# Kernel optimization log

Hardware: AMD Instinct MI355X
Metric: run time of the kernel (lower is better)

## Reference

```python
import jax, jax.numpy as jnp
import numpy as np

EPS = 1e-3  # Keras BatchNormalization default epsilon
ROWS = 14


def _lstm_step(h, c, x, W, U, b, act):
    # Keras gate order: i, f, g(cell), o
    z = x @ W + h @ U + b
    i, f, g, o = jnp.split(z, 4, axis=-1)
    c = jax.nn.sigmoid(f) * c + jax.nn.sigmoid(i) * act(g)
    h = jax.nn.sigmoid(o) * act(c)
    return h, c


def _lstm(xs, W, U, b, act):
    # xs: [B, T, F] -> (last_h, last_c), zero initial state
    B = xs.shape[0]
    D = U.shape[0]
    h0 = jnp.zeros((B, D), xs.dtype)
    c0 = jnp.zeros((B, D), xs.dtype)

    def step(carry, x):
        h, c = _lstm_step(carry[0], carry[1], x, W, U, b, act)
        return (h, c), h

    (h, c), hs = jax.lax.scan(step, (h0, c0), jnp.swapaxes(xs, 0, 1))
    return jnp.swapaxes(hs, 0, 1), h, c


def _bn(x, gamma, beta):
    # training-mode batchnorm over all axes but the last (channel) axis
    axes = tuple(range(x.ndim - 1))
    mean = jnp.mean(x, axis=axes)
    var = jnp.var(x, axis=axes)
    return (x - mean) * jax.lax.rsqrt(var + EPS) * gamma + beta


def setup_inputs() -> dict:
    key = jax.random.key(0)
    B, T, F = 65536, 32, 16
    D = 8   # lstm_forward_dims = output_dims * 2
    Do = 4  # lstm_backward_dims = output_dims
    ks = jax.random.split(key, 10)
    p = lambda k, shp: (0.1 * jax.random.normal(k, shp)).astype(jnp.float32)
    return {
        "noise_seed": jax.random.normal(ks[0], (B, T, F), dtype=jnp.float32),
        "W0": p(ks[1], (F, 4 * D)), "U0": p(ks[2], (D, 4 * D)), "b0": jnp.zeros((4 * D,), jnp.float32),
        "gamma_h": jnp.ones((D,), jnp.float32), "beta_h": jnp.zeros((D,), jnp.float32),
        "gamma_c": jnp.ones((D,), jnp.float32), "beta_c": jnp.zeros((D,), jnp.float32),
        "W1": p(ks[3], (D, 4 * D)), "U1": p(ks[4], (D, 4 * D)), "b1": jnp.zeros((4 * D,), jnp.float32),
        "gamma3": jnp.ones((D,), jnp.float32), "beta3": jnp.zeros((D,), jnp.float32),
        "W2": p(ks[5], (D, 4 * Do)), "U2": p(ks[6], (Do, 4 * Do)), "b2": jnp.zeros((4 * Do,), jnp.float32),
        "training": 1,
    }


def reference(noise_seed, W0, U0, b0, gamma_h, beta_h, gamma_c, beta_c,
              W1, U1, b1, gamma3, beta3, W2, U2, b2, training):
    # init LSTM (tanh activation), keep final states
    _, h, c = _lstm(noise_seed, W0, U0, b0, jnp.tanh)
    h = _bn(h, gamma_h, beta_h)
    c = _bn(c, gamma_c, beta_c)

    def step(carry, _):
        h, c = carry
        h2, c2 = _lstm_step(h, c, h, W1, U1, b1, jax.nn.relu)
        return (h2, c2), h2

    _, hs = jax.lax.scan(step, (h, c), None, length=ROWS)  # [ROWS, B, D]
    bars = jnp.swapaxes(hs[::-1], 0, 1)                    # reversed, [B, ROWS, D]
    bars = _bn(bars, gamma3, beta3)

    # backward LSTM (relu activation), return_sequences
    out, _, _ = _lstm(bars, W2, U2, b2, jax.nn.relu)       # [B, ROWS, Do]
    return out
```

## Files before the change

kernel.cpp:

```cpp
#include <hip/hip_runtime.h>
#include <hip/hip_bf16.h>

#define EPSV 1e-3f

__device__ __forceinline__ float rcp_fast(float x){ return __builtin_amdgcn_rcpf(x); }
__device__ __forceinline__ float sigm(float x){
    x = fminf(fmaxf(x, -30.f), 30.f);
    return rcp_fast(1.f + __expf(-x));
}
__device__ __forceinline__ float tanh_fast(float x){
    x = fminf(fmaxf(x, -15.f), 15.f);
    float e = __expf(2.f * x);
    return 1.f - 2.f * rcp_fast(e + 1.f);
}

template<int K>
__device__ __forceinline__ float bc8(float v){
    return __int_as_float(__builtin_amdgcn_ds_swizzle(__float_as_int(v), (K << 5) | 0x18));
}
#define BC8_ALL(dst, src) do { \
    dst[0]=bc8<0>(src); dst[1]=bc8<1>(src); dst[2]=bc8<2>(src); dst[3]=bc8<3>(src); \
    dst[4]=bc8<4>(src); dst[5]=bc8<5>(src); dst[6]=bc8<6>(src); dst[7]=bc8<7>(src); } while(0)

__global__ __launch_bounds__(256) void k1_lstm0(
    const float* __restrict__ noise, const float* __restrict__ W0,
    const float* __restrict__ U0, const float* __restrict__ b0,
    float* __restrict__ Hbuf, float* __restrict__ Cbuf, double* __restrict__ stats1)
{
    const int tid = threadIdx.x;
    const int d = tid & 7;
    const size_t b = (size_t)blockIdx.x * 32 + (tid >> 3);

    float w0c[16][4], u0c[8][4], b0v[4];
    #pragma unroll
    for (int g = 0; g < 4; ++g) b0v[g] = b0[8*g + d];
    #pragma unroll
    for (int f = 0; f < 16; ++f)
        #pragma unroll
        for (int g = 0; g < 4; ++g) w0c[f][g] = W0[f*32 + 8*g + d];
    #pragma unroll
    for (int e = 0; e < 8; ++e)
        #pragma unroll
        for (int g = 0; g < 4; ++g) u0c[e][g] = U0[e*32 + 8*g + d];

    const float4* __restrict__ xrow = reinterpret_cast<const float4*>(noise + b * 512);
    float h = 0.f, c = 0.f;
    #pragma unroll 2
    for (int t = 0; t < 32; ++t){
        float4 q0 = xrow[t*4+0], q1 = xrow[t*4+1], q2 = xrow[t*4+2], q3 = xrow[t*4+3];
        float hall[8]; BC8_ALL(hall, h);
        const float x[16] = {q0.x,q0.y,q0.z,q0.w, q1.x,q1.y,q1.z,q1.w,
                             q2.x,q2.y,q2.z,q2.w, q3.x,q3.y,q3.z,q3.w};
        float z[4] = {b0v[0], b0v[1], b0v[2], b0v[3]};
        #pragma unroll
        for (int f = 0; f < 16; ++f)
            #pragma unroll
            for (int g = 0; g < 4; ++g) z[g] = fmaf(x[f], w0c[f][g], z[g]);
        #pragma unroll
        for (int e = 0; e < 8; ++e)
            #pragma unroll
            for (int g = 0; g < 4; ++g) z[g] = fmaf(hall[e], u0c[e][g], z[g]);
        c = sigm(z[1])*c + sigm(z[0])*tanh_fast(z[2]);
        h = sigm(z[3])*tanh_fast(c);
    }
    Hbuf[(size_t)blockIdx.x*256 + tid] = h;
    Cbuf[(size_t)blockIdx.x*256 + tid] = c;

    float v0 = h, v1 = h*h, v2 = c, v3 = c*c;
    v0 += __shfl_down(v0,32); v0 += __shfl_down(v0,16); v0 += __shfl_down(v0,8);
    v1 += __shfl_down(v1,32); v1 += __shfl_down(v1,16); v1 += __shfl_down(v1,8);
    v2 += __shfl_down(v2,32); v2 += __shfl_down(v2,16); v2 += __shfl_down(v2,8);
    v3 += __shfl_down(v3,32); v3 += __shfl_down(v3,16); v3 += __shfl_down(v3,8);
    __shared__ float red[4][4][8];
    const int w = tid >> 6;
    if ((tid & 63) < 8){ red[0][w][d]=v0; red[1][w][d]=v1; red[2][w][d]=v2; red[3][w][d]=v3; }
    __syncthreads();
    if (tid < 32){
        const int s = tid >> 3, dd = tid & 7;
        float acc = red[s][0][dd] + red[s][1][dd] + red[s][2][dd] + red[s][3][dd];
        atomicAdd(stats1 + s*8 + dd, (double)acc);
    }
}

__global__ __launch_bounds__(256) void k2_ar(
    const float* __restrict__ Hbuf, const float* __restrict__ Cbuf,
    const double* __restrict__ stats1,
    const float* __restrict__ gamma_h, const float* __restrict__ beta_h,
    const float* __restrict__ gamma_c, const float* __restrict__ beta_c,
    const float* __restrict__ W1, const float* __restrict__ U1, const float* __restrict__ b1,
    double* __restrict__ stats3, int B)
{
    const int tid = threadIdx.x;
    const int d = tid & 7;
    const double invB = 1.0 / (double)B;
    const float meanH = (float)(stats1[d]      * invB);
    const float eH2   = (float)(stats1[8 + d]  * invB);
    const float meanC = (float)(stats1[16 + d] * invB);
    const float eC2   = (float)(stats1[24 + d] * invB);
    const float aH = gamma_h[d] * rsqrtf(eH2 - meanH*meanH + EPSV);
    const float aC = gamma_c[d] * rsqrtf(eC2 - meanC*meanC + EPSV);
    const float bH = beta_h[d] - meanH*aH;
    const float bC = beta_c[d] - meanC*aC;
    float h = fmaf(Hbuf[(size_t)blockIdx.x*256 + tid], aH, bH);
    float c = fmaf(Cbuf[(size_t)blockIdx.x*256 + tid], aC, bC);

    float wc[8][4], bcv[4];
    #pragma unroll
    for (int g = 0; g < 4; ++g) bcv[g] = b1[8*g + d];
    #pragma unroll
    for (int e = 0; e < 8; ++e)
        #pragma unroll
        for (int g = 0; g < 4; ++g) wc[e][g] = W1[e*32 + 8*g + d] + U1[e*32 + 8*g + d];

    float s1 = 0.f, s2 = 0.f;
    #pragma unroll
    for (int r = 0; r < 14; ++r){
        float hall[8]; BC8_ALL(hall, h);
        float z[4] = {bcv[0], bcv[1], bcv[2], bcv[3]};
        #pragma unroll
        for (int e = 0; e < 8; ++e)
            #pragma unroll
            for (int g = 0; g < 4; ++g) z[g] = fmaf(hall[e], wc[e][g], z[g]);
        c = sigm(z[1])*c + sigm(z[0])*fmaxf(z[2], 0.f);
        h = sigm(z[3])*fmaxf(c, 0.f);
        s1 += h; s2 = fmaf(h, h, s2);
    }
    s1 += __shfl_down(s1,32); s1 += __shfl_down(s1,16); s1 += __shfl_down(s1,8);
    s2 += __shfl_down(s2,32); s2 += __shfl_down(s2,16); s2 += __shfl_down(s2,8);
    __shared__ float red[2][4][8];
    const int w = tid >> 6;
    if ((tid & 63) < 8){ red[0][w][d] = s1; red[1][w][d] = s2; }
    __syncthreads();
    if (tid < 16){
        const int s = tid >> 3, dd = tid & 7;
        float acc = red[s][0][dd] + red[s][1][dd] + red[s][2][dd] + red[s][3][dd];
        atomicAdd(stats3 + s*8 + dd, (double)acc);
    }
}

__global__ __launch_bounds__(256) void k3_out(
    const float* __restrict__ Hbuf, const float* __restrict__ Cbuf,
    const double* __restrict__ stats1, const double* __restrict__ stats3,
    const float* __restrict__ gamma_h, const float* __restrict__ beta_h,
    const float* __restrict__ gamma_c, const float* __restrict__ beta_c,
    const float* __restrict__ W1, const float* __restrict__ U1, const float* __restrict__ b1,
    const float* __restrict__ gamma3, const float* __restrict__ beta3,
    const float* __restrict__ W2, const float* __restrict__ U2, const float* __restrict__ b2,
    float* __restrict__ out, int B)
{
    const int tid = threadIdx.x;
    const int d = tid & 7;
    const double invB = 1.0 / (double)B;
    const float meanH = (float)(stats1[d]      * invB);
    const float eH2   = (float)(stats1[8 + d]  * invB);
    const float meanC = (float)(stats1[16 + d] * invB);
    const float eC2   = (float)(stats1[24 + d] * invB);
    const float aH = gamma_h[d] * rsqrtf(eH2 - meanH*meanH + EPSV);
    const float aC = gamma_c[d] * rsqrtf(eC2 - meanC*meanC + EPSV);
    const float bH = beta_h[d] - meanH*aH;
    const float bC = beta_c[d] - meanC*aC;
    float h = fmaf(Hbuf[(size_t)blockIdx.x*256 + tid], aH, bH);
    float c = fmaf(Cbuf[(size_t)blockIdx.x*256 + tid], aC, bC);

    float wc[8][4], bcv[4];
    #pragma unroll
    for (int g = 0; g < 4; ++g) bcv[g] = b1[8*g + d];
    #pragma unroll
    for (int e = 0; e < 8; ++e)
        #pragma unroll
        for (int g = 0; g < 4; ++g) wc[e][g] = W1[e*32 + 8*g + d] + U1[e*32 + 8*g + d];

    float barh[14];
    #pragma unroll
    for (int r = 0; r < 14; ++r){
        float hall[8]; BC8_ALL(hall, h);
        float z[4] = {bcv[0], bcv[1], bcv[2], bcv[3]};
        #pragma unroll
        for (int e = 0; e < 8; ++e)
            #pragma unroll
            for (int g = 0; g < 4; ++g) z[g] = fmaf(hall[e], wc[e][g], z[g]);
        c = sigm(z[1])*c + sigm(z[0])*fmaxf(z[2], 0.f);
        h = sigm(z[3])*fmaxf(c, 0.f);
        barh[r] = h;
    }
    const double invN = 1.0 / ((double)B * 14.0);
    const float mean3 = (float)(stats3[d]     * invN);
    const float e32   = (float)(stats3[8 + d] * invN);
    const float a3 = gamma3[d] * rsqrtf(e32 - mean3*mean3 + EPSV);
    const float b3 = beta3[d] - mean3*a3;
    #pragma unroll
    for (int r = 0; r < 14; ++r) barh[r] = fmaf(barh[r], a3, b3);

    const int q = d & 3;
    float w2c[8][4], u2c[4][4], b2v[4];
    #pragma unroll
    for (int g = 0; g < 4; ++g) b2v[g] = b2[4*g + q];
    #pragma unroll
    for (int e = 0; e < 8; ++e)
        #pragma unroll
        for (int g = 0; g < 4; ++g) w2c[e][g] = W2[e*16 + 4*g + q];
    #pragma unroll
    for (int e = 0; e < 4; ++e)
        #pragma unroll
        for (int g = 0; g < 4; ++g) u2c[e][g] = U2[e*16 + 4*g + q];

    float ho = 0.f, co = 0.f;
    const size_t obase = ((size_t)blockIdx.x*32 + (tid >> 3)) * 56;
    #pragma unroll
    for (int r = 0; r < 14; ++r){
        const float cur = barh[13 - r];
        float be[8]; BC8_ALL(be, cur);
        float h4[4];
        h4[0]=bc8<0>(ho); h4[1]=bc8<1>(ho); h4[2]=bc8<2>(ho); h4[3]=bc8<3>(ho);
        float z[4] = {b2v[0], b2v[1], b2v[2], b2v[3]};
        #pragma unroll
        for (int e = 0; e < 8; ++e)
            #pragma unroll
            for (int g = 0; g < 4; ++g) z[g] = fmaf(be[e], w2c[e][g], z[g]);
        #pragma unroll
        for (int e = 0; e < 4; ++e)
            #pragma unroll
            for (int g = 0; g < 4; ++g) z[g] = fmaf(h4[e], u2c[e][g], z[g]);
        co = sigm(z[1])*co + sigm(z[0])*fmaxf(z[2], 0.f);
        ho = sigm(z[3])*fmaxf(co, 0.f);
        if (d < 4) out[obase + r*4 + d] = ho;
    }
}

extern "C" void kernel_launch(void* const* d_in, const int* in_sizes, int n_in,
                              void* d_out, int out_size, void* d_ws, size_t ws_size,
                              hipStream_t stream)
{
    const float* noise   = (const float*)d_in[0];
    const float* W0      = (const float*)d_in[1];
    const float* U0      = (const float*)d_in[2];
    const float* b0      = (const float*)d_in[3];
    const float* gamma_h = (const float*)d_in[4];
    const float* beta_h  = (const float*)d_in[5];
    const float* gamma_c = (const float*)d_in[6];
    const float* beta_c  = (const float*)d_in[7];
    const float* W1      = (const float*)d_in[8];
    const float* U1      = (const float*)d_in[9];
    const float* b1      = (const float*)d_in[10];
    const float* gamma3  = (const float*)d_in[11];
    const float* beta3   = (const float*)d_in[12];
    const float* W2      = (const float*)d_in[13];
    const float* U2      = (const float*)d_in[14];
    const float* b2      = (const float*)d_in[15];

    const int B = in_sizes[0] / (32 * 16);
    double* stats1 = (double*)d_ws;
    double* stats3 = stats1 + 32;
    float* Hbuf = (float*)((char*)d_ws + 512);
    float* Cbuf = Hbuf + (size_t)B * 8;

    hipMemsetAsync(d_ws, 0, 48 * sizeof(double), stream);
    const int nb = B / 32;
    k1_lstm0<<<nb, 256, 0, stream>>>(noise, W0, U0, b0, Hbuf, Cbuf, stats1);
    k2_ar<<<nb, 256, 0, stream>>>(Hbuf, Cbuf, stats1, gamma_h, beta_h, gamma_c, beta_c,
                                  W1, U1, b1, stats3, B);
    k3_out<<<nb, 256, 0, stream>>>(Hbuf, Cbuf, stats1, stats3, gamma_h, beta_h, gamma_c, beta_c,
                                   W1, U1, b1, gamma3, beta3, W2, U2, b2, (float*)d_out, B);
}
```

Baseline: 161.5 us.

## Split LSTM gates across lanes: one thread per gate column in k1 and k3

k1 and k3 now assign 32 lanes per sample, one per gate column, rather than 8 lanes each computing all four gates. Gate activations are exchanged with ds_swizzle and per-sample stats are pre-scaled by 0.25 to undo the 4x replication. The change cuts per-thread FMA work and register pressure and raises parallelism, with a launch bound of 4 and four times as many blocks. The cost is redundant input loads (each of the 32 lanes reads the full x row), more swizzles per step, and removal of input clamping in sigmoid.

```diff
diff --git a/kernel.cpp b/kernel.cpp
--- a/kernel.cpp
+++ b/kernel.cpp
@@ -5,14 +5,18 @@
 
 __device__ __forceinline__ float rcp_fast(float x){ return __builtin_amdgcn_rcpf(x); }
 __device__ __forceinline__ float sigm(float x){
-    x = fminf(fmaxf(x, -30.f), 30.f);
     return rcp_fast(1.f + __expf(-x));
 }
-__device__ __forceinline__ float tanh_fast(float x){
-    x = fminf(fmaxf(x, -15.f), 15.f);
-    float e = __expf(2.f * x);
-    return 1.f - 2.f * rcp_fast(e + 1.f);
-}
+
+#define KEEP(x) asm volatile("" : "+v"(x))
+
+template<int OR, int AND>
+__device__ __forceinline__ float swz(float v){
+    return __int_as_float(__builtin_amdgcn_ds_swizzle(__float_as_int(v), (OR << 5) | AND));
+}
+#define BCAST8(dst, src) do { \
+    dst[0]=swz<0,0x18>(src); dst[1]=swz<1,0x18>(src); dst[2]=swz<2,0x18>(src); dst[3]=swz<3,0x18>(src); \
+    dst[4]=swz<4,0x18>(src); dst[5]=swz<5,0x18>(src); dst[6]=swz<6,0x18>(src); dst[7]=swz<7,0x18>(src); } while(0)
 
 template<int K>
 __device__ __forceinline__ float bc8(float v){
@@ -22,63 +26,75 @@
     dst[0]=bc8<0>(src); dst[1]=bc8<1>(src); dst[2]=bc8<2>(src); dst[3]=bc8<3>(src); \
     dst[4]=bc8<4>(src); dst[5]=bc8<5>(src); dst[6]=bc8<6>(src); dst[7]=bc8<7>(src); } while(0)
 
-__global__ __launch_bounds__(256) void k1_lstm0(
+__global__ __launch_bounds__(256, 4) void k1_lstm0(
     const float* __restrict__ noise, const float* __restrict__ W0,
     const float* __restrict__ U0, const float* __restrict__ b0,
     float* __restrict__ Hbuf, float* __restrict__ Cbuf, double* __restrict__ stats1)
 {
     const int tid = threadIdx.x;
-    const int d = tid & 7;
-    const size_t b = (size_t)blockIdx.x * 32 + (tid >> 3);
-
-    float w0c[16][4], u0c[8][4], b0v[4];
-    #pragma unroll
-    for (int g = 0; g < 4; ++g) b0v[g] = b0[8*g + d];
-    #pragma unroll
-    for (int f = 0; f < 16; ++f)
-        #pragma unroll
-        for (int g = 0; g < 4; ++g) w0c[f][g] = W0[f*32 + 8*g + d];
-    #pragma unroll
-    for (int e = 0; e < 8; ++e)
-        #pragma unroll
-        for (int g = 0; g < 4; ++g) u0c[e][g] = U0[e*32 + 8*g + d];
-
-    const float4* __restrict__ xrow = reinterpret_cast<const float4*>(noise + b * 512);
-    float h = 0.f, c = 0.f;
+    const int col = tid & 31;
+    const int q   = tid & 7;
+    const int gt  = col >> 3;
+    const size_t s = (size_t)blockIdx.x * 8 + (tid >> 5);
+
+    float wcol[16], ucol[8];
+    #pragma unroll
+    for (int f = 0; f < 16; ++f) wcol[f] = W0[f*32 + col];
+    #pragma unroll
+    for (int e = 0; e < 8; ++e)  ucol[e] = U0[e*32 + col];
+    float bias = b0[col];
+    #pragma unroll
+    for (int f = 0; f < 16; ++f) KEEP(wcol[f]);
+    #pragma unroll
+    for (int e = 0; e < 8; ++e)  KEEP(ucol[e]);
+    KEEP(bias);
+    const float ckn = (gt == 2) ? -2.f : -1.f;
+    const float am  = (gt == 2) ?  2.f :  1.f;
+    const float an  = (gt == 2) ? -1.f :  0.f;
+
+    const float4* __restrict__ xrow = reinterpret_cast<const float4*>(noise + s * 512);
+    float h = 0.f, c = 0.f, hall[8];
+    #pragma unroll
+    for (int e = 0; e < 8; ++e) hall[e] = 0.f;
+
     #pragma unroll 2
     for (int t = 0; t < 32; ++t){
         float4 q0 = xrow[t*4+0], q1 = xrow[t*4+1], q2 = xrow[t*4+2], q3 = xrow[t*4+3];
-        float hall[8]; BC8_ALL(hall, h);
+        float z = bias;
+        #pragma unroll
+        for (int e = 0; e < 8; ++e) z = fmaf(hall[e], ucol[e], z);
         const float x[16] = {q0.x,q0.y,q0.z,q0.w, q1.x,q1.y,q1.z,q1.w,
                              q2.x,q2.y,q2.z,q2.w, q3.x,q3.y,q3.z,q3.w};
-        float z[4] = {b0v[0], b0v[1], b0v[2], b0v[3]};
-        #pragma unroll
-        for (int f = 0; f < 16; ++f)
-            #pragma unroll
-            for (int g = 0; g < 4; ++g) z[g] = fmaf(x[f], w0c[f][g], z[g]);
-        #pragma unroll
-        for (int e = 0; e < 8; ++e)
-            #pragma unroll
-            for (int g = 0; g < 4; ++g) z[g] = fmaf(hall[e], u0c[e][g], z[g]);
-        c = sigm(z[1])*c + sigm(z[0])*tanh_fast(z[2]);
-        h = sigm(z[3])*tanh_fast(c);
-    }
-    Hbuf[(size_t)blockIdx.x*256 + tid] = h;
-    Cbuf[(size_t)blockIdx.x*256 + tid] = c;
+        #pragma unroll
+        for (int f = 0; f < 16; ++f) z = fmaf(x[f], wcol[f], z);
+        const float a = fmaf(rcp_fast(1.f + __expf(z * ckn)), am, an);
+        const float ai = swz< 0,7>(a), af = swz< 8,7>(a), ag = swz<16,7>(a), ao = swz<24,7>(a);
+        c = fmaf(af, c, ai * ag);
+        const float s2 = rcp_fast(1.f + __expf(-2.f * c));
+        h = ao * (2.f * s2 - 1.f);
+        BCAST8(hall, h);
+    }
+    if (((tid >> 3) & 3) == 0){
+        Hbuf[s*8 + q] = h;
+        Cbuf[s*8 + q] = c;
+    }
 
     float v0 = h, v1 = h*h, v2 = c, v3 = c*c;
-    v0 += __shfl_down(v0,32); v0 += __shfl_down(v0,16); v0 += __shfl_down(v0,8);
-    v1 += __shfl_down(v1,32); v1 += __shfl_down(v1,16); v1 += __shfl_down(v1,8);
-    v2 += __shfl_down(v2,32); v2 += __shfl_down(v2,16); v2 += __shfl_down(v2,8);
-    v3 += __shfl_down(v3,32); v3 += __shfl_down(v3,16); v3 += __shfl_down(v3,8);
+    v0 += __shfl_xor(v0,8); v0 += __shfl_xor(v0,16); v0 += __shfl_xor(v0,32);
+    v1 += __shfl_xor(v1,8); v1 += __shfl_xor(v1,16); v1 += __shfl_xor(v1,32);
+    v2 += __shfl_xor(v2,8); v2 += __shfl_xor(v2,16); v2 += __shfl_xor(v2,32);
+    v3 += __shfl_xor(v3,8); v3 += __shfl_xor(v3,16); v3 += __shfl_xor(v3,32);
     __shared__ float red[4][4][8];
     const int w = tid >> 6;
-    if ((tid & 63) < 8){ red[0][w][d]=v0; red[1][w][d]=v1; red[2][w][d]=v2; red[3][w][d]=v3; }
+    if ((tid & 63) < 8){
+        red[0][w][q] = v0 * 0.25f; red[1][w][q] = v1 * 0.25f;
+        red[2][w][q] = v2 * 0.25f; red[3][w][q] = v3 * 0.25f;
+    }
     __syncthreads();
     if (tid < 32){
-        const int s = tid >> 3, dd = tid & 7;
-        float acc = red[s][0][dd] + red[s][1][dd] + red[s][2][dd] + red[s][3][dd];
-        atomicAdd(stats1 + s*8 + dd, (double)acc);
+        const int st = tid >> 3, dd = tid & 7;
+        float acc = red[st][0][dd] + red[st][1][dd] + red[st][2][dd] + red[st][3][dd];
+        atomicAdd(stats1 + st*8 + dd, (double)acc);
     }
 }
 
@@ -132,13 +148,13 @@
     if ((tid & 63) < 8){ red[0][w][d] = s1; red[1][w][d] = s2; }
     __syncthreads();
     if (tid < 16){
-        const int s = tid >> 3, dd = tid & 7;
-        float acc = red[s][0][dd] + red[s][1][dd] + red[s][2][dd] + red[s][3][dd];
-        atomicAdd(stats3 + s*8 + dd, (double)acc);
-    }
-}
-
-__global__ __launch_bounds__(256) void k3_out(
+        const int st = tid >> 3, dd = tid & 7;
+        float acc = red[st][0][dd] + red[st][1][dd] + red[st][2][dd] + red[st][3][dd];
+        atomicAdd(stats3 + st*8 + dd, (double)acc);
+    }
+}
+
+__global__ __launch_bounds__(256, 4) void k3_out(
     const float* __restrict__ Hbuf, const float* __restrict__ Cbuf,
     const double* __restrict__ stats1, const double* __restrict__ stats3,
     const float* __restrict__ gamma_h, const float* __restrict__ beta_h,
@@ -149,81 +165,85 @@
     float* __restrict__ out, int B)
 {
     const int tid = threadIdx.x;
-    const int d = tid & 7;
+    const int col = tid & 31;
+    const int q   = tid & 7;
+    const int gt  = col >> 3;
+    const size_t s = (size_t)blockIdx.x * 8 + (tid >> 5);
+
     const double invB = 1.0 / (double)B;
-    const float meanH = (float)(stats1[d]      * invB);
-    const float eH2   = (float)(stats1[8 + d]  * invB);
-    const float meanC = (float)(stats1[16 + d] * invB);
-    const float eC2   = (float)(stats1[24 + d] * invB);
-    const float aH = gamma_h[d] * rsqrtf(eH2 - meanH*meanH + EPSV);
-    const float aC = gamma_c[d] * rsqrtf(eC2 - meanC*meanC + EPSV);
-    const float bH = beta_h[d] - meanH*aH;
-    const float bC = beta_c[d] - meanC*aC;
-    float h = fmaf(Hbuf[(size_t)blockIdx.x*256 + tid], aH, bH);
-    float c = fmaf(Cbuf[(size_t)blockIdx.x*256 + tid], aC, bC);
-
-    float wc[8][4], bcv[4];
-    #pragma unroll
-    for (int g = 0; g < 4; ++g) bcv[g] = b1[8*g + d];
-    #pragma unroll
-    for (int e = 0; e < 8; ++e)
-        #pragma unroll
-        for (int g = 0; g < 4; ++g) wc[e][g] = W1[e*32 + 8*g + d] + U1[e*32 + 8*g + d];
-
+    const float meanH = (float)(stats1[q]      * invB);
+    const float eH2   = (float)(stats1[8 + q]  * invB);
+    const float meanC = (float)(stats1[16 + q] * invB);
+    const float eC2   = (float)(stats1[24 + q] * invB);
+    const float aH = gamma_h[q] * rsqrtf(eH2 - meanH*meanH + EPSV);
+    const float aC = gamma_c[q] * rsqrtf(eC2 - meanC*meanC + EPSV);
+    float h = fmaf(Hbuf[s*8 + q], aH, beta_h[q] - meanH*aH);
+    float c = fmaf(Cbuf[s*8 + q], aC, beta_c[q] - meanC*aC);
+
+    float wsum[8];
+    #pragma unroll
+    for (int e = 0; e < 8; ++e) wsum[e] = W1[e*32 + col] + U1[e*32 + col];
+    const float bias1 = b1[col];
+    const bool is_cell = (gt == 2);
+
+    float hall[8]; BCAST8(hall, h);
     float barh[14];
     #pragma unroll
     for (int r = 0; r < 14; ++r){
-        float hall[8]; BC8_ALL(hall, h);
-        float z[4] = {bcv[0], bcv[1], bcv[2], bcv[3]};
-        #pragma unroll
-        for (int e = 0; e < 8; ++e)
-            #pragma unroll
-            for (int g = 0; g < 4; ++g) z[g] = fmaf(hall[e], wc[e][g], z[g]);
-        c = sigm(z[1])*c + sigm(z[0])*fmaxf(z[2], 0.f);
-        h = sigm(z[3])*fmaxf(c, 0.f);
+        float z = bias1;
+        #pragma unroll
+        for (int e = 0; e < 8; ++e) z = fmaf(hall[e], wsum[e], z);
+        const float a = is_cell ? fmaxf(z, 0.f) : sigm(z);
+        const float ai = swz< 0,7>(a), af = swz< 8,7>(a), ag = swz<16,7>(a), ao = swz<24,7>(a);
+        c = fmaf(af, c, ai * ag);
+        h = ao * fmaxf(c, 0.f);
         barh[r] = h;
+        BCAST8(hall, h);
     }
     const double invN = 1.0 / ((double)B * 14.0);
-    const float mean3 = (float)(stats3[d]     * invN);
-    const float e32   = (float)(stats3[8 + d] * invN);
-    const float a3 = gamma3[d] * rsqrtf(e32 - mean3*mean3 + EPSV);
-    const float b3 = beta3[d] - mean3*a3;
+    const float mean3 = (float)(stats3[q]     * invN);
+    const float e32   = (float)(stats3[8 + q] * invN);
+    const float a3 = gamma3[q] * rsqrtf(e32 - mean3*mean3 + EPSV);
+    const float b3 = beta3[q] - mean3*a3;
     #pragma unroll
     for (int r = 0; r < 14; ++r) barh[r] = fmaf(barh[r], a3, b3);
 
-    const int q = d & 3;
-    float w2c[8][4], u2c[4][4], b2v[4];
-    #pragma unroll
-    for (int g = 0; g < 4; ++g) b2v[g] = b2[4*g + q];
-    #pragma unroll
-    for (int e = 0; e < 8; ++e)
-        #pragma unroll
-        for (int g = 0; g < 4; ++g) w2c[e][g] = W2[e*16 + 4*g + q];
-    #pragma unroll
-    for (int e = 0; e < 4; ++e)
-        #pragma unroll
-        for (int g = 0; g < 4; ++g) u2c[e][g] = U2[e*16 + 4*g + q];
+    const int col2 = tid & 15;
+    const int gt2  = col2 >> 2;
+    float w2col[8], u2col[4];
+    #pragma unroll
+    for (int e = 0; e < 8; ++e) w2col[e] = W2[e*16 + col2];
+    #pragma unroll
+    for (int e = 0; e < 4; ++e) u2col[e] = U2[e*16 + col2];
+    const float bias2 = b2[col2];
+    const bool is_cell2 = (gt2 == 2);
 
     float ho = 0.f, co = 0.f;
-    const size_t obase = ((size_t)blockIdx.x*32 + (tid >> 3)) * 56;
+    const size_t obase = s * 56;
     #pragma unroll
     for (int r = 0; r < 14; ++r){
-        const float cur = barh[13 - r];
-        float be[8]; BC8_ALL(be, cur);
-        float h4[4];
-        h4[0]=bc8<0>(ho); h4[1]=bc8<1>(ho); h4[2]=bc8<2>(ho); h4[3]=bc8<3>(ho);
-        float z[4] = {b2v[0], b2v[1], b2v[2], b2v[3]};
-        #pragma unroll
-        for (int e = 0; e < 8; ++e)
-            #pragma unroll
-            for (int g = 0; g < 4; ++g) z[g] = fmaf(be[e], w2c[e][g], z[g]);
-        #pragma unroll
-        for (int e = 0; e < 4; ++e)
-            #pragma unroll
-            for (int g = 0; g < 4; ++g) z[g] = fmaf(h4[e], u2c[e][g], z[g]);
-        co = sigm(z[1])*co + sigm(z[0])*fmaxf(z[2], 0.f);
-        ho = sigm(z[3])*fmaxf(co, 0.f);
-        if (d < 4) out[obase + r*4 + d] = ho;
+        float z = bias2;
+        #pragma unroll
+        for (int e = 0; e < 8; ++e){
+            float be;
+            if (e==0) be=swz<0,0x18>(barh[13-r]); else if (e==1) be=swz<1,0x18>(barh[13-r]);
+            else if (e==2) be=swz<2,0x18>(barh[13-r]); else if (e==3) be=swz<3,0x18>(barh[13-r]);
+            else if (e==4) be=swz<4,0x18>(barh[13-r]); else if (e==5) be=swz<5,0x18>(barh[13-r]);
+            else if (e==6) be=swz<6,0x18>(barh[13-r]); else be=swz<7,0x18>(barh[13-r]);
+            z = fmaf(be, w2col[e], z);
+        }
+        {
+            const float h0v = swz<0,0x10>(ho), h1v = swz<1,0x10>(ho),
+                        h2v = swz<2,0x10>(ho), h3v = swz<3,0x10>(ho);
+            z = fmaf(h0v, u2col[0], z); z = fmaf(h1v, u2col[1], z);
+            z = fmaf(h2v, u2col[2], z); z = fmaf(h3v, u2col[3], z);
+        }
+        const float a = is_cell2 ? fmaxf(z, 0.f) : sigm(z);
+        const float ai = swz< 0,0x13>(a), af = swz< 4,0x13>(a),
+                    ag = swz< 8,0x13>(a), ao = swz<12,0x13>(a);
+        co = fmaf(af, co, ai * ag);
+        ho = ao * fmaxf(co, 0.f);
+        if ((tid & 31) < 4) out[obase + r*4 + (tid & 3)] = ho;
     }
 }
 
@@ -255,10 +275,9 @@
     float* Cbuf = Hbuf + (size_t)B * 8;
 
     hipMemsetAsync(d_ws, 0, 48 * sizeof(double), stream);
-    const int nb = B / 32;
-    k1_lstm0<<<nb, 256, 0, stream>>>(noise, W0, U0, b0, Hbuf, Cbuf, stats1);
-    k2_ar<<<nb, 256, 0, stream>>>(Hbuf, Cbuf, stats1, gamma_h, beta_h, gamma_c, beta_c,
-                                  W1, U1, b1, stats3, B);
-    k3_out<<<nb, 256, 0, stream>>>(Hbuf, Cbuf, stats1, stats3, gamma_h, beta_h, gamma_c, beta_c,
-                                   W1, U1, b1, gamma3, beta3, W2, U2, b2, (float*)d_out, B);
-}
+    k1_lstm0<<<B/8, 256, 0, stream>>>(noise, W0, U0, b0, Hbuf, Cbuf, stats1);
+    k2_ar<<<B/32, 256, 0, stream>>>(Hbuf, Cbuf, stats1, gamma_h, beta_h, gamma_c, beta_c,
+                                    W1, U1, b1, stats3, B);
+    k3_out<<<B/8, 256, 0, stream>>>(Hbuf, Cbuf, stats1, stats3, gamma_h, beta_h, gamma_c, beta_c,
+                                    W1, U1, b1, gamma3, beta3, W2, U2, b2, (float*)d_out, B);
+}
```

Result: slower. 293.2 us (+81.5%).
